# Optimization experiments

Measured on AMD Instinct MI355X. Metric: run time of the kernel, lower is better.

Reference implementation:

```python
import jax, jax.numpy as jnp
import numpy as np

N_NODES = 50000


def setup_inputs() -> dict:
    key = jax.random.key(0)
    k1, k2, k3, k4 = jax.random.split(key, 4)
    N, E, F_IN, F_OUT = N_NODES, 1600000, 512, 128
    x = jax.random.normal(k1, (N, F_IN), dtype=jnp.float32)
    edge_index = jax.random.randint(k2, (2, E), 0, N, dtype=jnp.int64)
    edge_weight = jax.random.uniform(k3, (E,), dtype=jnp.float32)
    # glorot init for weight, zeros bias (as in the original layer)
    limit = np.sqrt(6.0 / (F_IN + F_OUT)).astype(np.float32)
    weight = jax.random.uniform(k4, (F_IN, F_OUT), dtype=jnp.float32,
                                minval=-limit, maxval=limit)
    bias = jnp.zeros((F_OUT,), dtype=jnp.float32)
    return {"x": x, "edge_index": edge_index, "edge_weight": edge_weight,
            "weight": weight, "bias": bias}


def reference(x, edge_index, edge_weight, weight, bias):
    # dropout rate is 0 in this config -> identity
    h = x @ weight                                # [N, F_out] dense transform
    src, dst = edge_index[0], edge_index[1]
    # support @ h : sparse adjacency aggregation (SpMM) via gather + segment_sum
    msgs = h[src] * edge_weight[:, None]          # [E, F_out]
    agg = jax.ops.segment_sum(msgs, dst, num_segments=N_NODES)  # [N, F_out]
    return jax.nn.relu(agg + bias)
```

## Files before the change

### kernel.cpp

```cpp
#include <hip/hip_runtime.h>

#define F_IN  512
#define F_OUT 128
#define CB    128
#define EPB   4096
#define CMAX  512
#define CAP   4096

typedef __attribute__((ext_vector_type(8))) short  short8;
typedef __attribute__((ext_vector_type(4))) float  floatx4;

__device__ __forceinline__ unsigned short f2bf(float f) {
    unsigned u = __float_as_uint(f);
    return (unsigned short)((u + 0x7FFF + ((u >> 16) & 1)) >> 16);
}
__device__ __forceinline__ float bf2f(unsigned b) {
    return __uint_as_float(b << 16);
}

__global__ __launch_bounds__(256) void hist_convert(
    const int* __restrict__ ei, int* __restrict__ cnt, int E, int C, int FB,
    const float* __restrict__ w, unsigned short* __restrict__ wt)
{
    const int tid = threadIdx.x;
    if ((int)blockIdx.x >= FB) {
        int cid = blockIdx.x - FB;
        int g0  = cid * 512 + tid;
        #pragma unroll
        for (int r = 0; r < 2; ++r) {
            int gid = g0 + r * 256;
            int n = gid >> 9, k = gid & 511;
            wt[gid] = f2bf(w[(size_t)k * F_OUT + n]);
        }
        return;
    }
    __shared__ int lh[CMAX];
    lh[tid] = 0; lh[tid + 256] = 0;
    __syncthreads();
    int base = blockIdx.x * EPB;
    #pragma unroll
    for (int j = 0; j < EPB / 256; ++j) {
        int e = base + j * 256 + tid;
        if (e < E) atomicAdd(&lh[ei[E + e] >> 7], 1);
    }
    __syncthreads();
    if (tid < C && lh[tid] > 0) atomicAdd(&cnt[tid], lh[tid]);
    int t2 = tid + 256;
    if (t2 < C && lh[t2] > 0) atomicAdd(&cnt[t2], lh[t2]);
}

__global__ __launch_bounds__(512) void scan_bins(
    const int* __restrict__ cnt, int* __restrict__ binoff,
    int* __restrict__ cursor, int C, int E)
{
    __shared__ int s[CMAX];
    int tid = threadIdx.x;
    int v = (tid < C) ? cnt[tid] : 0;
    s[tid] = v;
    __syncthreads();
    #pragma unroll
    for (int off = 1; off < CMAX; off <<= 1) {
        int t = (tid >= off) ? s[tid - off] : 0;
        __syncthreads();
        s[tid] += t;
        __syncthreads();
    }
    if (tid < C) { int ex = s[tid] - v; binoff[tid] = ex; cursor[tid] = ex; }
    if (tid == 0) binoff[C] = E;
}

__global__ __launch_bounds__(256, 2) void fill_gemm(
    const int* __restrict__ ei, const float* __restrict__ ew,
    int* __restrict__ cursor, uint2* __restrict__ ent, int E, int C, int FB,
    const float* __restrict__ x, const unsigned short* __restrict__ wt,
    unsigned short* __restrict__ h, int N)
{
    const int tid = threadIdx.x;

    if ((int)blockIdx.x < FB) {
        __shared__ int lh[CMAX];
        __shared__ int lbase[CMAX];
        lh[tid] = 0; lh[tid + 256] = 0;
        __syncthreads();

        const int base = blockIdx.x * EPB;
        unsigned       mykey[EPB / 256];
        unsigned char  mydl[EPB / 256];
        short          mybin[EPB / 256];
        unsigned short myrank[EPB / 256];

        #pragma unroll
        for (int j = 0; j < EPB / 256; ++j) {
            int e = base + j * 256 + tid;
            mybin[j] = -1;
            if (e < E) {
                int   src = ei[e];
                int   dst = ei[E + e];
                float w   = ew[e];
                int bin = dst >> 7;
                mykey[j]  = (unsigned)src | ((unsigned)f2bf(w) << 16);
                mydl[j]   = (unsigned char)(dst & (CB - 1));
                mybin[j]  = (short)bin;
                myrank[j] = (unsigned short)atomicAdd(&lh[bin], 1);
            }
        }
        __syncthreads();
        if (tid < C && lh[tid] > 0) lbase[tid] = atomicAdd(&cursor[tid], lh[tid]);
        int t2 = tid + 256;
        if (t2 < C && lh[t2] > 0) lbase[t2] = atomicAdd(&cursor[t2], lh[t2]);
        __syncthreads();
        #pragma unroll
        for (int j = 0; j < EPB / 256; ++j) {
            if (mybin[j] >= 0) {
                int p = lbase[mybin[j]] + myrank[j];
                ent[p] = make_uint2(mykey[j], mydl[j]);
            }
        }
        return;
    }

    __shared__ unsigned short sa[64 * 68];
    __shared__ unsigned short sb[128 * 68];

    const int wave = tid >> 6, lane = tid & 63;
    const int g    = lane >> 4, l16 = lane & 15;
    const int m0   = (blockIdx.x - FB) * 64;

    const int arow = tid >> 2, aq = tid & 3;
    const int brow = tid >> 1, bh = tid & 1;

    floatx4 acc[8];
    #pragma unroll
    for (int i = 0; i < 8; ++i) acc[i] = (floatx4)(0.f);

    const bool  avalid = (m0 + arow) < N;
    const float* xp = x + (size_t)(m0 + arow) * F_IN + aq * 16;
    const unsigned short* bp = wt + brow * F_IN + bh * 32;

    float4 ax[4];
    uint4  bv[4];
    #pragma unroll
    for (int i = 0; i < 4; ++i) ax[i] = make_float4(0.f, 0.f, 0.f, 0.f);
    if (avalid) {
        #pragma unroll
        for (int i = 0; i < 4; ++i) ax[i] = ((const float4*)xp)[i];
    }
    #pragma unroll
    for (int i = 0; i < 4; ++i) bv[i] = ((const uint4*)bp)[i];

    for (int s = 0; s < 8; ++s) {
        __syncthreads();
        #pragma unroll
        for (int i = 0; i < 4; ++i) {
            ushort4 t;
            t.x = f2bf(ax[i].x); t.y = f2bf(ax[i].y);
            t.z = f2bf(ax[i].z); t.w = f2bf(ax[i].w);
            *(ushort4*)&sa[arow * 68 + aq * 16 + i * 4] = t;
        }
        #pragma unroll
        for (int i = 0; i < 4; ++i) {
            *(uint2*)&sb[brow * 68 + bh * 32 + i * 8]     = make_uint2(bv[i].x, bv[i].y);
            *(uint2*)&sb[brow * 68 + bh * 32 + i * 8 + 4] = make_uint2(bv[i].z, bv[i].w);
        }
        if (s < 7) {
            int k0n = (s + 1) * 64;
            if (avalid) {
                #pragma unroll
                for (int i = 0; i < 4; ++i) ax[i] = ((const float4*)(xp + k0n))[i];
            }
            #pragma unroll
            for (int i = 0; i < 4; ++i) bv[i] = ((const uint4*)(bp + k0n))[i];
        }
        __syncthreads();

        #pragma unroll
        for (int kc = 0; kc < 2; ++kc) {
            union { ushort4 u[2]; short8 v; } af;
            int abase = (wave * 16 + l16) * 68 + kc * 32 + g * 8;
            af.u[0] = *(ushort4*)&sa[abase];
            af.u[1] = *(ushort4*)&sa[abase + 4];
            #pragma unroll
            for (int nt = 0; nt < 8; ++nt) {
                union { ushort4 u[2]; short8 v; } bf;
                int bbase = (nt * 16 + l16) * 68 + kc * 32 + g * 8;
                bf.u[0] = *(ushort4*)&sb[bbase];
                bf.u[1] = *(ushort4*)&sb[bbase + 4];
                acc[nt] = __builtin_amdgcn_mfma_f32_16x16x32_bf16(af.v, bf.v, acc[nt], 0, 0, 0);
            }
        }
    }

    #pragma unroll
    for (int nt = 0; nt < 8; ++nt) {
        #pragma unroll
        for (int r = 0; r < 4; ++r) {
            int row = m0 + wave * 16 + g * 4 + r;
            if (row < N) h[(size_t)row * F_OUT + nt * 16 + l16] = f2bf(acc[nt][r]);
        }
    }
}

__global__ __launch_bounds__(256) void fine_agg(
    const unsigned short* __restrict__ h, const uint2* __restrict__ ent,
    const int* __restrict__ binoff, const float* __restrict__ bias,
    float* __restrict__ out, int N)
{
    __shared__ unsigned ssort[CAP];
    __shared__ int lh[64], lcur[64];
    __shared__ int sso[65];

    const int b     = blockIdx.x;
    const int cb    = b >> 1;
    const int hb    = b & 1;
    const int tid   = threadIdx.x;
    const int start = binoff[cb];
    const int end   = binoff[cb + 1];
    const int wave  = tid >> 6;
    const int lane  = tid & 63;
    const int half  = lane >> 5;
    const int q     = lane & 31;
    const float4 bv = *(const float4*)&bias[q * 4];

    if (tid < 64) lh[tid] = 0;
    __syncthreads();

    for (int i = start + tid; i < end; i += 256) {
        int d = (int)ent[i].y;
        if ((d >> 6) == hb) atomicAdd(&lh[d & 63], 1);
    }
    __syncthreads();

    if (wave == 0) {
        int v = lh[lane & 63];
        int orig = v;
        #pragma unroll
        for (int off = 1; off < 64; off <<= 1) {
            int t = __shfl_up(v, off);
            if (lane >= off) v += t;
        }
        sso[lane]  = v - orig;
        lcur[lane] = v - orig;
        if (lane == 63) sso[64] = v;
    }
    __syncthreads();
    const int hcnt = sso[64];

    if (hcnt <= CAP) {
        for (int i = start + tid; i < end; i += 256) {
            uint2 e = ent[i];
            int d = (int)e.y;
            if ((d >> 6) == hb) {
                int r = atomicAdd(&lcur[d & 63], 1);
                ssort[r] = e.x;
            }
        }
        __syncthreads();

        #pragma unroll 1
        for (int t = 0; t < 16; ++t) {
            int nd   = wave * 16 + t;
            int node = cb * CB + hb * 64 + nd;
            int s = sso[nd], e = sso[nd + 1];
            float4 acc = make_float4(0.f, 0.f, 0.f, 0.f);
            for (int i = s; i < e; i += 8) {
                #pragma unroll
                for (int j = 0; j < 4; ++j) {
                    int idx = i + j * 2 + half;
                    unsigned bk = 0;
                    if (idx < e) bk = ssort[idx];
                    float wgt = bf2f(bk >> 16);
                    uint2 hv = *(const uint2*)&h[(size_t)(bk & 0xFFFF) * F_OUT + q * 4];
                    acc.x += bf2f(hv.x & 0xFFFF) * wgt;
                    acc.y += bf2f(hv.x >> 16)    * wgt;
                    acc.z += bf2f(hv.y & 0xFFFF) * wgt;
                    acc.w += bf2f(hv.y >> 16)    * wgt;
                }
            }
            acc.x += __shfl_xor(acc.x, 32);
            acc.y += __shfl_xor(acc.y, 32);
            acc.z += __shfl_xor(acc.z, 32);
            acc.w += __shfl_xor(acc.w, 32);
            if (half == 0 && node < N) {
                float4 o;
                o.x = fmaxf(acc.x + bv.x, 0.f);
                o.y = fmaxf(acc.y + bv.y, 0.f);
                o.z = fmaxf(acc.z + bv.z, 0.f);
                o.w = fmaxf(acc.w + bv.w, 0.f);
                *(float4*)&out[(size_t)node * F_OUT + q * 4] = o;
            }
        }
    } else {
        #pragma unroll 1
        for (int t = 0; t < 16; ++t) {
            int nd   = wave * 16 + t;
            int node = cb * CB + hb * 64 + nd;
            int want = hb * 64 + nd;
            float4 acc = make_float4(0.f, 0.f, 0.f, 0.f);
            for (int i = start; i < end; ++i) {
                uint2 e = ent[i];
                if ((int)e.y == want) {
                    unsigned bk = e.x;
                    float wgt = bf2f(bk >> 16);
                    uint2 hv = *(const uint2*)&h[(size_t)(bk & 0xFFFF) * F_OUT + q * 4];
                    acc.x += bf2f(hv.x & 0xFFFF) * wgt;
                    acc.y += bf2f(hv.x >> 16)    * wgt;
                    acc.z += bf2f(hv.y & 0xFFFF) * wgt;
                    acc.w += bf2f(hv.y >> 16)    * wgt;
                }
            }
            if (half == 0 && node < N) {
                float4 o;
                o.x = fmaxf(acc.x + bv.x, 0.f);
                o.y = fmaxf(acc.y + bv.y, 0.f);
                o.z = fmaxf(acc.z + bv.z, 0.f);
                o.w = fmaxf(acc.w + bv.w, 0.f);
                *(float4*)&out[(size_t)node * F_OUT + q * 4] = o;
            }
        }
    }
}

static inline size_t align256(size_t x) { return (x + 255) & ~(size_t)255; }

extern "C" void kernel_launch(void* const* d_in, const int* in_sizes, int n_in,
                              void* d_out, int out_size, void* d_ws, size_t ws_size,
                              hipStream_t stream)
{
    const float* x    = (const float*)d_in[0];
    const int*   ei   = (const int*)  d_in[1];
    const float* ew   = (const float*)d_in[2];
    const float* w    = (const float*)d_in[3];
    const float* bias = (const float*)d_in[4];
    float*       out  = (float*)d_out;

    const int N = in_sizes[0] / F_IN;
    const int E = in_sizes[2];
    const int C = (N + CB - 1) / CB;

    char*  ws = (char*)d_ws;
    size_t off = 0;
    unsigned short* h      = (unsigned short*)(ws + off); off += align256((size_t)N * F_OUT * 2);
    unsigned short* wt     = (unsigned short*)(ws + off); off += align256((size_t)F_OUT * F_IN * 2);
    int*            cnt    = (int*)(ws + off);            off += align256((size_t)(C + 1) * 4);
    int*            binoff = (int*)(ws + off);            off += align256((size_t)(C + 1) * 4);
    int*            cursor = (int*)(ws + off);            off += align256((size_t)C * 4);
    uint2*          ent    = (uint2*)(ws + off);          off += align256((size_t)E * 8);

    const int FB = (E + EPB - 1) / EPB;
    const int GB = (N + 63) / 64;
    const int WB = (F_IN * F_OUT) / 512;

    (void)hipMemsetAsync(cnt, 0, (size_t)C * 4, stream);
    hist_convert<<<FB + WB, 256, 0, stream>>>(ei, cnt, E, C, FB, w, wt);
    scan_bins<<<1, 512, 0, stream>>>(cnt, binoff, cursor, C, E);
    fill_gemm<<<FB + GB, 256, 0, stream>>>(ei, ew, cursor, ent, E, C, FB,
                                           x, wt, h, N);
    fine_agg<<<2 * C, 256, 0, stream>>>(h, ent, binoff, bias, out, N);
}
```

Before: 275.0 us.

## Replace histogram+scan binning with fixed-capacity per-bin slabs of 32 nodes

Removes the separate histogram pass, the single-block scan kernel and the memset. Edges now go into fixed-capacity slabs (2048 entries per 32-node bin), with offsets taken from per-bin atomic cursors. This avoids one full read of the destination indices and two launches, and fine_agg now handles one bin of 32 nodes per block. In exchange the workspace grows, and the bins are more numerous, so each fill block loops over about 1600 shared counters and issues more global atomics. Overflowing bins fall back to a very slow full scan of all edges.

```diff
diff --git a/kernel.cpp b/kernel.cpp
--- a/kernel.cpp
+++ b/kernel.cpp
@@ -2,10 +2,10 @@
 
 #define F_IN  512
 #define F_OUT 128
-#define CB    128
+#define FBIN  32
 #define EPB   4096
-#define CMAX  512
-#define CAP   4096
+#define C2MAX 1600
+#define CAPF  2048
 
 typedef __attribute__((ext_vector_type(8))) short  short8;
 typedef __attribute__((ext_vector_type(4))) float  floatx4;
@@ -18,69 +18,38 @@
     return __uint_as_float(b << 16);
 }
 
-__global__ __launch_bounds__(256) void hist_convert(
-    const int* __restrict__ ei, int* __restrict__ cnt, int E, int C, int FB,
-    const float* __restrict__ w, unsigned short* __restrict__ wt)
+__global__ __launch_bounds__(256) void prep(
+    const float* __restrict__ w, unsigned short* __restrict__ wt,
+    int* __restrict__ cursor, int C2)
 {
     const int tid = threadIdx.x;
-    if ((int)blockIdx.x >= FB) {
-        int cid = blockIdx.x - FB;
-        int g0  = cid * 512 + tid;
+    if ((int)blockIdx.x < 128) {
+        int g0 = blockIdx.x * 512 + tid;
         #pragma unroll
         for (int r = 0; r < 2; ++r) {
             int gid = g0 + r * 256;
             int n = gid >> 9, k = gid & 511;
             wt[gid] = f2bf(w[(size_t)k * F_OUT + n]);
         }
-        return;
-    }
-    __shared__ int lh[CMAX];
-    lh[tid] = 0; lh[tid + 256] = 0;
-    __syncthreads();
-    int base = blockIdx.x * EPB;
-    #pragma unroll
-    for (int j = 0; j < EPB / 256; ++j) {
-        int e = base + j * 256 + tid;
-        if (e < E) atomicAdd(&lh[ei[E + e] >> 7], 1);
-    }
-    __syncthreads();
-    if (tid < C && lh[tid] > 0) atomicAdd(&cnt[tid], lh[tid]);
-    int t2 = tid + 256;
-    if (t2 < C && lh[t2] > 0) atomicAdd(&cnt[t2], lh[t2]);
-}
-
-__global__ __launch_bounds__(512) void scan_bins(
-    const int* __restrict__ cnt, int* __restrict__ binoff,
-    int* __restrict__ cursor, int C, int E)
-{
-    __shared__ int s[CMAX];
-    int tid = threadIdx.x;
-    int v = (tid < C) ? cnt[tid] : 0;
-    s[tid] = v;
-    __syncthreads();
-    #pragma unroll
-    for (int off = 1; off < CMAX; off <<= 1) {
-        int t = (tid >= off) ? s[tid - off] : 0;
-        __syncthreads();
-        s[tid] += t;
-        __syncthreads();
-    }
-    if (tid < C) { int ex = s[tid] - v; binoff[tid] = ex; cursor[tid] = ex; }
-    if (tid == 0) binoff[C] = E;
+    } else {
+        int c = ((int)blockIdx.x - 128) * 256 + tid;
+        if (c < C2) cursor[c] = 0;
+    }
 }
 
 __global__ __launch_bounds__(256, 2) void fill_gemm(
     const int* __restrict__ ei, const float* __restrict__ ew,
-    int* __restrict__ cursor, uint2* __restrict__ ent, int E, int C, int FB,
+    int* __restrict__ cursor, uint2* __restrict__ ent, int E, int C2, int FB,
     const float* __restrict__ x, const unsigned short* __restrict__ wt,
     unsigned short* __restrict__ h, int N)
 {
+    __shared__ __align__(16) char smem[(64 * 68 + 128 * 68) * 2];
     const int tid = threadIdx.x;
 
     if ((int)blockIdx.x < FB) {
-        __shared__ int lh[CMAX];
-        __shared__ int lbase[CMAX];
-        lh[tid] = 0; lh[tid + 256] = 0;
+        int* lh    = (int*)smem;
+        int* lbase = (int*)smem + C2MAX;
+        for (int c = tid; c < C2; c += 256) lh[c] = 0;
         __syncthreads();
 
         const int base = blockIdx.x * EPB;
@@ -97,34 +66,34 @@
                 int   src = ei[e];
                 int   dst = ei[E + e];
                 float w   = ew[e];
-                int bin = dst >> 7;
+                int bin = dst >> 5;
                 mykey[j]  = (unsigned)src | ((unsigned)f2bf(w) << 16);
-                mydl[j]   = (unsigned char)(dst & (CB - 1));
+                mydl[j]   = (unsigned char)(dst & (FBIN - 1));
                 mybin[j]  = (short)bin;
                 myrank[j] = (unsigned short)atomicAdd(&lh[bin], 1);
             }
         }
         __syncthreads();
-        if (tid < C && lh[tid] > 0) lbase[tid] = atomicAdd(&cursor[tid], lh[tid]);
-        int t2 = tid + 256;
-        if (t2 < C && lh[t2] > 0) lbase[t2] = atomicAdd(&cursor[t2], lh[t2]);
+        for (int c = tid; c < C2; c += 256)
+            if (lh[c] > 0) lbase[c] = atomicAdd(&cursor[c], lh[c]);
         __syncthreads();
         #pragma unroll
         for (int j = 0; j < EPB / 256; ++j) {
             if (mybin[j] >= 0) {
-                int p = lbase[mybin[j]] + myrank[j];
-                ent[p] = make_uint2(mykey[j], mydl[j]);
+                int o = lbase[mybin[j]] + myrank[j];
+                if (o < CAPF)
+                    ent[(size_t)(int)mybin[j] * CAPF + o] = make_uint2(mykey[j], mydl[j]);
             }
         }
         return;
     }
 
-    __shared__ unsigned short sa[64 * 68];
-    __shared__ unsigned short sb[128 * 68];
+    unsigned short* sa = (unsigned short*)smem;
+    unsigned short* sb = sa + 64 * 68;
 
     const int wave = tid >> 6, lane = tid & 63;
     const int g    = lane >> 4, l16 = lane & 15;
-    const int m0   = (blockIdx.x - FB) * 64;
+    const int m0   = ((int)blockIdx.x - FB) * 64;
 
     const int arow = tid >> 2, aq = tid & 3;
     const int brow = tid >> 1, bh = tid & 1;
@@ -202,72 +171,66 @@
 
 __global__ __launch_bounds__(256) void fine_agg(
     const unsigned short* __restrict__ h, const uint2* __restrict__ ent,
-    const int* __restrict__ binoff, const float* __restrict__ bias,
-    float* __restrict__ out, int N)
+    const int* __restrict__ cursor, const float* __restrict__ bias,
+    float* __restrict__ out, int N, int E,
+    const int* __restrict__ ei, const float* __restrict__ ew)
 {
-    __shared__ unsigned ssort[CAP];
-    __shared__ int lh[64], lcur[64];
-    __shared__ int sso[65];
-
-    const int b     = blockIdx.x;
-    const int cb    = b >> 1;
-    const int hb    = b & 1;
-    const int tid   = threadIdx.x;
-    const int start = binoff[cb];
-    const int end   = binoff[cb + 1];
-    const int wave  = tid >> 6;
-    const int lane  = tid & 63;
-    const int half  = lane >> 5;
-    const int q     = lane & 31;
+    __shared__ unsigned ssort[CAPF];
+    __shared__ int lh[FBIN], lcur[FBIN];
+    __shared__ int sso[FBIN + 1];
+
+    const int b    = blockIdx.x;
+    const int tid  = threadIdx.x;
+    const int wave = tid >> 6;
+    const int lane = tid & 63;
+    const int half = lane >> 5;
+    const int q    = lane & 31;
     const float4 bv = *(const float4*)&bias[q * 4];
-
-    if (tid < 64) lh[tid] = 0;
+    const int raw  = cursor[b];
+    const int cnt  = raw < CAPF ? raw : CAPF;
+    const uint2* slab = ent + (size_t)b * CAPF;
+
+    if (tid < FBIN) lh[tid] = 0;
     __syncthreads();
 
-    for (int i = start + tid; i < end; i += 256) {
-        int d = (int)ent[i].y;
-        if ((d >> 6) == hb) atomicAdd(&lh[d & 63], 1);
-    }
+    for (int i = tid; i < cnt; i += 256)
+        atomicAdd(&lh[(int)slab[i].y], 1);
     __syncthreads();
 
-    if (wave == 0) {
-        int v = lh[lane & 63];
+    if (wave == 0 && lane < FBIN) {
+        int v = lh[lane];
         int orig = v;
         #pragma unroll
-        for (int off = 1; off < 64; off <<= 1) {
+        for (int off = 1; off < FBIN; off <<= 1) {
             int t = __shfl_up(v, off);
             if (lane >= off) v += t;
         }
         sso[lane]  = v - orig;
         lcur[lane] = v - orig;
-        if (lane == 63) sso[64] = v;
+        if (lane == FBIN - 1) sso[FBIN] = v;
     }
     __syncthreads();
-    const int hcnt = sso[64];
-
-    if (hcnt <= CAP) {
-        for (int i = start + tid; i < end; i += 256) {
-            uint2 e = ent[i];
-            int d = (int)e.y;
-            if ((d >> 6) == hb) {
-                int r = atomicAdd(&lcur[d & 63], 1);
-                ssort[r] = e.x;
-            }
+
+    if (raw <= CAPF) {
+        for (int i = tid; i < cnt; i += 256) {
+            uint2 e = slab[i];
+            int r = atomicAdd(&lcur[(int)e.y], 1);
+            ssort[r] = e.x;
         }
         __syncthreads();
 
         #pragma unroll 1
-        for (int t = 0; t < 16; ++t) {
-            int nd   = wave * 16 + t;
-            int node = cb * CB + hb * 64 + nd;
-            int s = sso[nd], e = sso[nd + 1];
+        for (int t = 0; t < 8; ++t) {
+            int nd   = wave * 8 + t;
+            int node = b * FBIN + nd;
+            int s = sso[nd], e2 = sso[nd + 1];
             float4 acc = make_float4(0.f, 0.f, 0.f, 0.f);
-            for (int i = s; i < e; i += 8) {
+            for (int i = s; i < e2; i += 8) {
                 #pragma unroll
                 for (int j = 0; j < 4; ++j) {
                     int idx = i + j * 2 + half;
                     unsigned bk = 0;
-                    if (idx < e) bk = ssort[idx];
+                    if (idx < e2) bk = ssort[idx];
                     float wgt = bf2f(bk >> 16);
                     uint2 hv = *(const uint2*)&h[(size_t)(bk & 0xFFFF) * F_OUT + q * 4];
                     acc.x += bf2f(hv.x & 0xFFFF) * wgt;
@@ -291,23 +254,24 @@
         }
     } else {
         #pragma unroll 1
-        for (int t = 0; t < 16; ++t) {
-            int nd   = wave * 16 + t;
-            int node = cb * CB + hb * 64 + nd;
-            int want = hb * 64 + nd;
+        for (int t = 0; t < 8; ++t) {
+            int nd   = wave * 8 + t;
+            int node = b * FBIN + nd;
             float4 acc = make_float4(0.f, 0.f, 0.f, 0.f);
-            for (int i = start; i < end; ++i) {
-                uint2 e = ent[i];
-                if ((int)e.y == want) {
-                    unsigned bk = e.x;
-                    float wgt = bf2f(bk >> 16);
-                    uint2 hv = *(const uint2*)&h[(size_t)(bk & 0xFFFF) * F_OUT + q * 4];
+            for (int e = half; e < E; e += 2) {
+                if (ei[E + e] == node) {
+                    float wgt = ew[e];
+                    uint2 hv = *(const uint2*)&h[(size_t)ei[e] * F_OUT + q * 4];
                     acc.x += bf2f(hv.x & 0xFFFF) * wgt;
                     acc.y += bf2f(hv.x >> 16)    * wgt;
                     acc.z += bf2f(hv.y & 0xFFFF) * wgt;
                     acc.w += bf2f(hv.y >> 16)    * wgt;
                 }
             }
+            acc.x += __shfl_xor(acc.x, 32);
+            acc.y += __shfl_xor(acc.y, 32);
+            acc.z += __shfl_xor(acc.z, 32);
+            acc.w += __shfl_xor(acc.w, 32);
             if (half == 0 && node < N) {
                 float4 o;
                 o.x = fmaxf(acc.x + bv.x, 0.f);
@@ -333,27 +297,23 @@
     const float* bias = (const float*)d_in[4];
     float*       out  = (float*)d_out;
 
-    const int N = in_sizes[0] / F_IN;
-    const int E = in_sizes[2];
-    const int C = (N + CB - 1) / CB;
+    const int N  = in_sizes[0] / F_IN;
+    const int E  = in_sizes[2];
+    const int C2 = (N + FBIN - 1) / FBIN;
 
     char*  ws = (char*)d_ws;
     size_t off = 0;
     unsigned short* h      = (unsigned short*)(ws + off); off += align256((size_t)N * F_OUT * 2);
     unsigned short* wt     = (unsigned short*)(ws + off); off += align256((size_t)F_OUT * F_IN * 2);
-    int*            cnt    = (int*)(ws + off);            off += align256((size_t)(C + 1) * 4);
-    int*            binoff = (int*)(ws + off);            off += align256((size_t)(C + 1) * 4);
-    int*            cursor = (int*)(ws + off);            off += align256((size_t)C * 4);
-    uint2*          ent    = (uint2*)(ws + off);          off += align256((size_t)E * 8);
+    int*            cursor = (int*)(ws + off);            off += align256((size_t)C2 * 4);
+    uint2*          ent    = (uint2*)(ws + off);          off += align256((size_t)C2 * CAPF * 8);
 
     const int FB = (E + EPB - 1) / EPB;
     const int GB = (N + 63) / 64;
-    const int WB = (F_IN * F_OUT) / 512;
-
-    (void)hipMemsetAsync(cnt, 0, (size_t)C * 4, stream);
-    hist_convert<<<FB + WB, 256, 0, stream>>>(ei, cnt, E, C, FB, w, wt);
-    scan_bins<<<1, 512, 0, stream>>>(cnt, binoff, cursor, C, E);
-    fill_gemm<<<FB + GB, 256, 0, stream>>>(ei, ew, cursor, ent, E, C, FB,
+    const int ZB = (C2 + 255) / 256;
+
+    prep<<<128 + ZB, 256, 0, stream>>>(w, wt, cursor, C2);
+    fill_gemm<<<FB + GB, 256, 0, stream>>>(ei, ew, cursor, ent, E, C2, FB,
                                            x, wt, h, N);
-    fine_agg<<<2 * C, 256, 0, stream>>>(h, ent, binoff, bias, out, N);
-}
+    fine_agg<<<C2, 256, 0, stream>>>(h, ent, cursor, bias, out, N, E, ei, ew);
+}
```

Measured after the change: 252.2 us. 1.09x faster.
